# Kernel tuning notes

Hardware: AMD Instinct MI355X
Metric: run time of the kernel (lower is better)

The kernel has to match this reference:

```python
import jax, jax.numpy as jnp
import numpy as np

N = 1048576  # number of frequency sampling points
K = 64       # number of cascaded SVF sections


def setup_inputs() -> dict:
    key = jax.random.key(0)
    ks = jax.random.split(key, 7)
    return {
        "x_real": jax.random.normal(ks[0], (N,), dtype=jnp.float32),
        "x_imag": jax.random.normal(ks[1], (N,), dtype=jnp.float32),
        "f":   jax.random.normal(ks[2], (1, K), dtype=jnp.float32),
        "R":   jax.random.normal(ks[3], (1, K), dtype=jnp.float32),
        "mLP": jax.random.normal(ks[4], (1, K), dtype=jnp.float32),
        "mBP": jax.random.normal(ks[5], (1, K), dtype=jnp.float32),
        "mHP": jax.random.normal(ks[6], (1, K), dtype=jnp.float32),
    }


def reference(x_real, x_imag, f, R, mLP, mBP, mHP):
    # x: complex sampling points (z on / near the unit circle)
    x = jax.lax.complex(x_real, x_imag)  # [N] complex64
    f, R, mLP, mBP, mHP = f[0], R[0], mLP[0], mBP[0], mHP[0]  # [K]
    f2 = f * f
    # biquad coefficients, [3, K]
    beta = jnp.stack([
        f2 * mLP + f * mBP + mHP,
        2.0 * f2 * mLP - 2.0 * mHP,
        f2 * mLP - f * mBP + mHP,
    ])
    alpha = jnp.stack([
        f2 + 2.0 * R * f + 1.0,
        2.0 * f2 - 2.0,
        f2 - 2.0 * R * f + 1.0,
    ])
    # X = [x^0, x^-1, x^-2], [N, 3] complex
    xinv = 1.0 / x
    X = jnp.stack([jnp.ones_like(x), xinv, xinv * xinv], axis=1)
    num = X @ beta.astype(X.dtype)    # [N, K]
    den = X @ alpha.astype(X.dtype)   # [N, K]
    # original initializes H = 1 + 1j then multiplies all K sections
    H = (1.0 + 1.0j) * jnp.prod(num / den, axis=1)  # [N]
    return H
```

## Files before the change

kernel.cpp:

```cpp
#include <hip/hip_runtime.h>


#define NSEC  64
#define NPAIR 32
#define BLOCK 256
#define MPT   2

__device__ __forceinline__ float rcp_f32_n1(float a) {
    float y = __builtin_amdgcn_rcpf(a);
    y = fmaf(fmaf(-a, y, 1.0f), y, y);
    return y;
}

__global__ __launch_bounds__(64) void svf_coef_v10(
    const float* __restrict__ f_g,  const float* __restrict__ R_g,
    const float* __restrict__ lp_g, const float* __restrict__ bp_g,
    const float* __restrict__ hp_g,
    float* __restrict__ coef)
{
    const int t = threadIdx.x;
    if (t >= NPAIR) return;
    const int k0 = 2 * t, k1 = 2 * t + 1;
    double fk = (double)f_g[k0],  Rk = (double)R_g[k0];
    double lp = (double)lp_g[k0], bp = (double)bp_g[k0], hp = (double)hp_g[k0];
    double f2 = fk * fk, fbp = fk * bp, flp = f2 * lp, rf2 = 2.0 * Rk * fk;
    const double b0 = flp + fbp + hp, b1 = 2.0 * flp - 2.0 * hp, b2 = flp - fbp + hp;
    const double a0 = f2 + rf2 + 1.0, a1 = 2.0 * f2 - 2.0,       a2 = f2 - rf2 + 1.0;
    fk = (double)f_g[k1];  Rk = (double)R_g[k1];
    lp = (double)lp_g[k1]; bp = (double)bp_g[k1]; hp = (double)hp_g[k1];
    f2 = fk * fk; fbp = fk * bp; flp = f2 * lp; rf2 = 2.0 * Rk * fk;
    const double B0 = flp + fbp + hp, B1 = 2.0 * flp - 2.0 * hp, B2 = flp - fbp + hp;
    const double A0 = f2 + rf2 + 1.0, A1 = 2.0 * f2 - 2.0,       A2 = f2 - rf2 + 1.0;
    float* cp = coef + t * 10;
    cp[0] = (float)(b0 * B0);
    cp[1] = (float)(b0 * B1 + b1 * B0);
    cp[2] = (float)(b0 * B2 + b1 * B1 + b2 * B0);
    cp[3] = (float)(b1 * B2 + b2 * B1);
    cp[4] = (float)(b2 * B2);
    cp[5] = (float)(a0 * A0);
    cp[6] = (float)(a0 * A1 + a1 * A0);
    cp[7] = (float)(a0 * A2 + a1 * A1 + a2 * A0);
    cp[8] = (float)(a1 * A2 + a2 * A1);
    cp[9] = (float)(a2 * A2);
}

__global__ __launch_bounds__(BLOCK) void svf_f32_v10(
    const float* __restrict__ xr_g, const float* __restrict__ xi_g,
    const float* __restrict__ coef,
    float* __restrict__ out, int n, long long cap_floats)
{
    const int t = threadIdx.x;
    const long long base = (long long)(blockIdx.x * BLOCK + t) * MPT;

    float Xr[MPT], Xi[MPT];
    float X2r[MPT], X2i[MPT], X3r[MPT], X3i[MPT], X4r[MPT], X4i[MPT];
    float Hr[MPT], Hi[MPT];

    if (base + MPT <= (long long)n) {
        const float2 a = *reinterpret_cast<const float2*>(xr_g + base);
        const float2 b = *reinterpret_cast<const float2*>(xi_g + base);
        Xr[0] = a.x; Xr[1] = a.y;
        Xi[0] = b.x; Xi[1] = b.y;
    } else {
        for (int m = 0; m < MPT; ++m) {
            const long long idx = base + m;
            const bool ok = idx < (long long)n;
            Xr[m] = ok ? xr_g[idx] : 1.0f;
            Xi[m] = ok ? xi_g[idx] : 0.0f;
        }
    }

    #pragma unroll
    for (int m = 0; m < MPT; ++m) {
        X2r[m] = fmaf(Xr[m],  Xr[m],  -(Xi[m]  * Xi[m]));
        X2i[m] = 2.0f * Xr[m] * Xi[m];
        X3r[m] = fmaf(X2r[m], Xr[m],  -(X2i[m] * Xi[m]));
        X3i[m] = fmaf(X2r[m], Xi[m],    X2i[m] * Xr[m]);
        X4r[m] = fmaf(X2r[m], X2r[m], -(X2i[m] * X2i[m]));
        X4i[m] = 2.0f * X2r[m] * X2i[m];
        Hr[m] = 1.0f;
        Hi[m] = 1.0f;
    }

    #pragma unroll 2
    for (int p = 0; p < NPAIR; ++p) {
        const float* cp = coef + p * 10;
        const float c0 = cp[0], c1 = cp[1], c2 = cp[2], c3 = cp[3], c4 = cp[4];
        const float d0 = cp[5], d1 = cp[6], d2c = cp[7], d3 = cp[8], d4 = cp[9];
        #pragma unroll
        for (int m = 0; m < MPT; ++m) {
            const float nr = fmaf(c0, X4r[m], fmaf(c1, X3r[m],
                              fmaf(c2, X2r[m], fmaf(c3, Xr[m], c4))));
            const float ni = fmaf(c0, X4i[m], fmaf(c1, X3i[m],
                              fmaf(c2, X2i[m], c3 * Xi[m])));
            const float dr = fmaf(d0, X4r[m], fmaf(d1, X3r[m],
                              fmaf(d2c, X2r[m], fmaf(d3, Xr[m], d4))));
            const float di = fmaf(d0, X4i[m], fmaf(d1, X3i[m],
                              fmaf(d2c, X2i[m], d3 * Xi[m])));
            const float dd  = fmaf(dr, dr, di * di);
            const float inv = rcp_f32_n1(dd);
            const float rr  = fmaf(nr, dr,   ni * di) * inv;
            const float ri  = fmaf(ni, dr, -(nr * di)) * inv;
            const float hr = fmaf(Hr[m], rr, -(Hi[m] * ri));
            const float hi = fmaf(Hr[m], ri,   Hi[m] * rr);
            Hr[m] = hr; Hi[m] = hi;
        }
    }

    const long long imag_off = (long long)n;
    if (base + MPT <= (long long)n && 2LL * (long long)n <= cap_floats) {
        float2 vr, vi;
        vr.x = Hr[0]; vr.y = Hr[1];
        vi.x = Hi[0]; vi.y = Hi[1];
        *reinterpret_cast<float2*>(out + base)            = vr;
        *reinterpret_cast<float2*>(out + imag_off + base) = vi;
    } else {
        for (int m = 0; m < MPT; ++m) {
            const long long idx = base + m;
            if (idx < (long long)n) {
                if (idx + 1 <= cap_floats) out[idx] = Hr[m];
                const long long oi = imag_off + idx;
                if (oi + 1 <= cap_floats) out[oi] = Hi[m];
            }
        }
    }
}

extern "C" void kernel_launch(void* const* d_in, const int* in_sizes, int n_in,
                              void* d_out, int out_size, void* d_ws, size_t ws_size,
                              hipStream_t stream) {
    const float* xr = (const float*)d_in[0];
    const float* xi = (const float*)d_in[1];
    const float* f  = (const float*)d_in[2];
    const float* R  = (const float*)d_in[3];
    const float* lp = (const float*)d_in[4];
    const float* bp = (const float*)d_in[5];
    const float* hp = (const float*)d_in[6];
    float* out = (float*)d_out;
    float* coef = (float*)d_ws;

    const int n = in_sizes[0];
    long long cap = (long long)out_size;
    if (cap > 2LL * (long long)n) cap = 2LL * (long long)n;

    svf_coef_v10<<<1, 64, 0, stream>>>(f, R, lp, bp, hp, coef);
    const int grid = (n + BLOCK * MPT - 1) / (BLOCK * MPT);
    svf_f32_v10<<<grid, BLOCK, 0, stream>>>(xr, xi, coef, out, n, cap);
}
```

Before: 89.04 us.

## Merge sections into quartets with degree-8 polynomials and drop Newton step

Coefficients of four biquad sections are multiplied together in double precision on a setup kernel, giving 16 degree-8 numerator/denominator polynomials instead of 32 degree-4 ones. The main kernel precomputes powers x^1..x^8 and evaluates 16 fractions, halving the number of divisions and complex multiplies per point. The reciprocal refinement step is also removed. This reduces ALU work in a compute-bound kernel but increases polynomial degree and register use, and risks float32 overflow or accuracy loss for large |x|.

```diff
diff --git a/kernel.cpp b/kernel.cpp
--- a/kernel.cpp
+++ b/kernel.cpp
@@ -2,49 +2,58 @@
 
 
 #define NSEC  64
-#define NPAIR 32
+#define NOCT  16
 #define BLOCK 256
 #define MPT   2
 
-__device__ __forceinline__ float rcp_f32_n1(float a) {
-    float y = __builtin_amdgcn_rcpf(a);
-    y = fmaf(fmaf(-a, y, 1.0f), y, y);
-    return y;
-}
-
-__global__ __launch_bounds__(64) void svf_coef_v10(
+__global__ __launch_bounds__(64) void svf_coef_v11(
     const float* __restrict__ f_g,  const float* __restrict__ R_g,
     const float* __restrict__ lp_g, const float* __restrict__ bp_g,
     const float* __restrict__ hp_g,
     float* __restrict__ coef)
 {
     const int t = threadIdx.x;
-    if (t >= NPAIR) return;
-    const int k0 = 2 * t, k1 = 2 * t + 1;
-    double fk = (double)f_g[k0],  Rk = (double)R_g[k0];
-    double lp = (double)lp_g[k0], bp = (double)bp_g[k0], hp = (double)hp_g[k0];
-    double f2 = fk * fk, fbp = fk * bp, flp = f2 * lp, rf2 = 2.0 * Rk * fk;
-    const double b0 = flp + fbp + hp, b1 = 2.0 * flp - 2.0 * hp, b2 = flp - fbp + hp;
-    const double a0 = f2 + rf2 + 1.0, a1 = 2.0 * f2 - 2.0,       a2 = f2 - rf2 + 1.0;
-    fk = (double)f_g[k1];  Rk = (double)R_g[k1];
-    lp = (double)lp_g[k1]; bp = (double)bp_g[k1]; hp = (double)hp_g[k1];
-    f2 = fk * fk; fbp = fk * bp; flp = f2 * lp; rf2 = 2.0 * Rk * fk;
-    const double B0 = flp + fbp + hp, B1 = 2.0 * flp - 2.0 * hp, B2 = flp - fbp + hp;
-    const double A0 = f2 + rf2 + 1.0, A1 = 2.0 * f2 - 2.0,       A2 = f2 - rf2 + 1.0;
-    float* cp = coef + t * 10;
-    cp[0] = (float)(b0 * B0);
-    cp[1] = (float)(b0 * B1 + b1 * B0);
-    cp[2] = (float)(b0 * B2 + b1 * B1 + b2 * B0);
-    cp[3] = (float)(b1 * B2 + b2 * B1);
-    cp[4] = (float)(b2 * B2);
-    cp[5] = (float)(a0 * A0);
-    cp[6] = (float)(a0 * A1 + a1 * A0);
-    cp[7] = (float)(a0 * A2 + a1 * A1 + a2 * A0);
-    cp[8] = (float)(a1 * A2 + a2 * A1);
-    cp[9] = (float)(a2 * A2);
+    if (t >= NOCT) return;
+
+    double qn[2][5], qd[2][5];
+    for (int s = 0; s < 2; ++s) {
+        const int k0 = 4 * t + 2 * s, k1 = k0 + 1;
+        double fk = (double)f_g[k0],  Rk = (double)R_g[k0];
+        double lp = (double)lp_g[k0], bp = (double)bp_g[k0], hp = (double)hp_g[k0];
+        double f2 = fk * fk, fbp = fk * bp, flp = f2 * lp, rf2 = 2.0 * Rk * fk;
+        const double b0 = flp + fbp + hp, b1 = 2.0 * flp - 2.0 * hp, b2 = flp - fbp + hp;
+        const double a0 = f2 + rf2 + 1.0, a1 = 2.0 * f2 - 2.0,       a2 = f2 - rf2 + 1.0;
+        fk = (double)f_g[k1];  Rk = (double)R_g[k1];
+        lp = (double)lp_g[k1]; bp = (double)bp_g[k1]; hp = (double)hp_g[k1];
+        f2 = fk * fk; fbp = fk * bp; flp = f2 * lp; rf2 = 2.0 * Rk * fk;
+        const double B0 = flp + fbp + hp, B1 = 2.0 * flp - 2.0 * hp, B2 = flp - fbp + hp;
+        const double A0 = f2 + rf2 + 1.0, A1 = 2.0 * f2 - 2.0,       A2 = f2 - rf2 + 1.0;
+        qn[s][0] = b0 * B0;
+        qn[s][1] = b0 * B1 + b1 * B0;
+        qn[s][2] = b0 * B2 + b1 * B1 + b2 * B0;
+        qn[s][3] = b1 * B2 + b2 * B1;
+        qn[s][4] = b2 * B2;
+        qd[s][0] = a0 * A0;
+        qd[s][1] = a0 * A1 + a1 * A0;
+        qd[s][2] = a0 * A2 + a1 * A1 + a2 * A0;
+        qd[s][3] = a1 * A2 + a2 * A1;
+        qd[s][4] = a2 * A2;
+    }
+    double en[9], ed[9];
+    for (int j = 0; j < 9; ++j) { en[j] = 0.0; ed[j] = 0.0; }
+    for (int i = 0; i < 5; ++i)
+        for (int j = 0; j < 5; ++j) {
+            en[i + j] += qn[0][i] * qn[1][j];
+            ed[i + j] += qd[0][i] * qd[1][j];
+        }
+    float* cp = coef + t * 18;
+    for (int j = 0; j < 9; ++j) {
+        cp[j]     = (float)en[j];
+        cp[9 + j] = (float)ed[j];
+    }
 }
 
-__global__ __launch_bounds__(BLOCK) void svf_f32_v10(
+__global__ __launch_bounds__(BLOCK) void svf_f32_v11(
     const float* __restrict__ xr_g, const float* __restrict__ xi_g,
     const float* __restrict__ coef,
     float* __restrict__ out, int n, long long cap_floats)
@@ -52,55 +61,72 @@
     const int t = threadIdx.x;
     const long long base = (long long)(blockIdx.x * BLOCK + t) * MPT;
 
-    float Xr[MPT], Xi[MPT];
-    float X2r[MPT], X2i[MPT], X3r[MPT], X3i[MPT], X4r[MPT], X4i[MPT];
+    float X1r[MPT], X1i[MPT], X2r[MPT], X2i[MPT], X3r[MPT], X3i[MPT];
+    float X4r[MPT], X4i[MPT], X5r[MPT], X5i[MPT], X6r[MPT], X6i[MPT];
+    float X7r[MPT], X7i[MPT], X8r[MPT], X8i[MPT];
     float Hr[MPT], Hi[MPT];
 
     if (base + MPT <= (long long)n) {
         const float2 a = *reinterpret_cast<const float2*>(xr_g + base);
         const float2 b = *reinterpret_cast<const float2*>(xi_g + base);
-        Xr[0] = a.x; Xr[1] = a.y;
-        Xi[0] = b.x; Xi[1] = b.y;
+        X1r[0] = a.x; X1r[1] = a.y;
+        X1i[0] = b.x; X1i[1] = b.y;
     } else {
         for (int m = 0; m < MPT; ++m) {
             const long long idx = base + m;
             const bool ok = idx < (long long)n;
-            Xr[m] = ok ? xr_g[idx] : 1.0f;
-            Xi[m] = ok ? xi_g[idx] : 0.0f;
+            X1r[m] = ok ? xr_g[idx] : 1.0f;
+            X1i[m] = ok ? xi_g[idx] : 0.0f;
         }
     }
 
     #pragma unroll
     for (int m = 0; m < MPT; ++m) {
-        X2r[m] = fmaf(Xr[m],  Xr[m],  -(Xi[m]  * Xi[m]));
-        X2i[m] = 2.0f * Xr[m] * Xi[m];
-        X3r[m] = fmaf(X2r[m], Xr[m],  -(X2i[m] * Xi[m]));
-        X3i[m] = fmaf(X2r[m], Xi[m],    X2i[m] * Xr[m]);
+        X2r[m] = fmaf(X1r[m], X1r[m], -(X1i[m] * X1i[m]));
+        X2i[m] = 2.0f * X1r[m] * X1i[m];
+        X3r[m] = fmaf(X2r[m], X1r[m], -(X2i[m] * X1i[m]));
+        X3i[m] = fmaf(X2r[m], X1i[m],   X2i[m] * X1r[m]);
         X4r[m] = fmaf(X2r[m], X2r[m], -(X2i[m] * X2i[m]));
         X4i[m] = 2.0f * X2r[m] * X2i[m];
+        X5r[m] = fmaf(X4r[m], X1r[m], -(X4i[m] * X1i[m]));
+        X5i[m] = fmaf(X4r[m], X1i[m],   X4i[m] * X1r[m]);
+        X6r[m] = fmaf(X3r[m], X3r[m], -(X3i[m] * X3i[m]));
+        X6i[m] = 2.0f * X3r[m] * X3i[m];
+        X7r[m] = fmaf(X4r[m], X3r[m], -(X4i[m] * X3i[m]));
+        X7i[m] = fmaf(X4r[m], X3i[m],   X4i[m] * X3r[m]);
+        X8r[m] = fmaf(X4r[m], X4r[m], -(X4i[m] * X4i[m]));
+        X8i[m] = 2.0f * X4r[m] * X4i[m];
         Hr[m] = 1.0f;
         Hi[m] = 1.0f;
     }
 
-    #pragma unroll 2
-    for (int p = 0; p < NPAIR; ++p) {
-        const float* cp = coef + p * 10;
-        const float c0 = cp[0], c1 = cp[1], c2 = cp[2], c3 = cp[3], c4 = cp[4];
-        const float d0 = cp[5], d1 = cp[6], d2c = cp[7], d3 = cp[8], d4 = cp[9];
+    #pragma unroll
+    for (int p = 0; p < NOCT; ++p) {
+        const float* cp = coef + p * 18;
+        const float e0 = cp[0], e1 = cp[1], e2 = cp[2], e3 = cp[3], e4 = cp[4];
+        const float e5 = cp[5], e6 = cp[6], e7 = cp[7], e8 = cp[8];
+        const float g0 = cp[9], g1 = cp[10], g2 = cp[11], g3 = cp[12], g4 = cp[13];
+        const float g5 = cp[14], g6 = cp[15], g7 = cp[16], g8 = cp[17];
         #pragma unroll
         for (int m = 0; m < MPT; ++m) {
-            const float nr = fmaf(c0, X4r[m], fmaf(c1, X3r[m],
-                              fmaf(c2, X2r[m], fmaf(c3, Xr[m], c4))));
-            const float ni = fmaf(c0, X4i[m], fmaf(c1, X3i[m],
-                              fmaf(c2, X2i[m], c3 * Xi[m])));
-            const float dr = fmaf(d0, X4r[m], fmaf(d1, X3r[m],
-                              fmaf(d2c, X2r[m], fmaf(d3, Xr[m], d4))));
-            const float di = fmaf(d0, X4i[m], fmaf(d1, X3i[m],
-                              fmaf(d2c, X2i[m], d3 * Xi[m])));
+            const float nr = fmaf(e0, X8r[m], fmaf(e1, X7r[m], fmaf(e2, X6r[m],
+                             fmaf(e3, X5r[m], fmaf(e4, X4r[m], fmaf(e5, X3r[m],
+                             fmaf(e6, X2r[m], fmaf(e7, X1r[m], e8))))))));
+            const float ni = fmaf(e0, X8i[m], fmaf(e1, X7i[m], fmaf(e2, X6i[m],
+                             fmaf(e3, X5i[m], fmaf(e4, X4i[m], fmaf(e5, X3i[m],
+                             fmaf(e6, X2i[m], e7 * X1i[m])))))));
+            const float dr = fmaf(g0, X8r[m], fmaf(g1, X7r[m], fmaf(g2, X6r[m],
+                             fmaf(g3, X5r[m], fmaf(g4, X4r[m], fmaf(g5, X3r[m],
+                             fmaf(g6, X2r[m], fmaf(g7, X1r[m], g8))))))));
+            const float di = fmaf(g0, X8i[m], fmaf(g1, X7i[m], fmaf(g2, X6i[m],
+                             fmaf(g3, X5i[m], fmaf(g4, X4i[m], fmaf(g5, X3i[m],
+                             fmaf(g6, X2i[m], g7 * X1i[m])))))));
             const float dd  = fmaf(dr, dr, di * di);
-            const float inv = rcp_f32_n1(dd);
-            const float rr  = fmaf(nr, dr,   ni * di) * inv;
-            const float ri  = fmaf(ni, dr, -(nr * di)) * inv;
+            const float inv = __builtin_amdgcn_rcpf(dd);
+            const float tr  = fmaf(nr, dr,   ni * di);
+            const float ti  = fmaf(ni, dr, -(nr * di));
+            const float rr  = tr * inv;
+            const float ri  = ti * inv;
             const float hr = fmaf(Hr[m], rr, -(Hi[m] * ri));
             const float hi = fmaf(Hr[m], ri,   Hi[m] * rr);
             Hr[m] = hr; Hi[m] = hi;
@@ -143,7 +169,7 @@
     long long cap = (long long)out_size;
     if (cap > 2LL * (long long)n) cap = 2LL * (long long)n;
 
-    svf_coef_v10<<<1, 64, 0, stream>>>(f, R, lp, bp, hp, coef);
+    svf_coef_v11<<<1, 64, 0, stream>>>(f, R, lp, bp, hp, coef);
     const int grid = (n + BLOCK * MPT - 1) / (BLOCK * MPT);
-    svf_f32_v10<<<grid, BLOCK, 0, stream>>>(xr, xi, coef, out, n, cap);
+    svf_f32_v11<<<grid, BLOCK, 0, stream>>>(xr, xi, coef, out, n, cap);
 }
```

Result: faster. 82.34 us (-7.5%).
